# Optimization experiments

Measured on AMD Instinct MI355X. Metric: run time of the kernel, lower is better.

## Reference

```python
import jax, jax.numpy as jnp
import numpy as np

N_EMBD = 1024
N_HEAD = 16
B, T = 4, 2048


def setup_inputs() -> dict:
    key = jax.random.key(0)
    ks = jax.random.split(key, 9)
    s = 1.0 / np.sqrt(N_EMBD)
    def lin(k):
        kw, kb = jax.random.split(k)
        W = jax.random.uniform(kw, (N_EMBD, N_EMBD), jnp.float32, -s, s)
        b = jax.random.uniform(kb, (N_EMBD,), jnp.float32, -s, s)
        return W, b
    Wq, bq = lin(ks[0])
    Wk, bk = lin(ks[1])
    Wv, bv = lin(ks[2])
    Wc, bc = lin(ks[3])
    x = jax.random.normal(ks[4], (B, T, N_EMBD), jnp.float32)
    return {"x": x, "Wq": Wq, "bq": bq, "Wk": Wk, "bk": bk,
            "Wv": Wv, "bv": bv, "Wc": Wc, "bc": bc}


def reference(x, Wq, bq, Wk, bk, Wv, bv, Wc, bc):
    Bsz, Tlen, C = x.shape
    hd = C // N_HEAD  # head dim
    # projections (torch Linear: x @ W.T + b)
    q = x @ Wq.T + bq
    k = x @ Wk.T + bk
    v = x @ Wv.T + bv
    # [B, H, T, hd]
    q = q.reshape(Bsz, Tlen, N_HEAD, hd).transpose(0, 2, 1, 3)
    k = k.reshape(Bsz, Tlen, N_HEAD, hd).transpose(0, 2, 1, 3)
    v = v.reshape(Bsz, Tlen, N_HEAD, hd).transpose(0, 2, 1, 3)
    scale = 1.0 / np.sqrt(hd).astype(np.float32)
    att = jnp.einsum('bhqd,bhkd->bhqk', q, k) * scale  # [B,H,T,T]
    causal = jnp.tril(jnp.ones((Tlen, Tlen), dtype=bool))
    att = jnp.where(causal[None, None, :, :], att, -jnp.inf)
    att = jax.nn.softmax(att, axis=-1)
    y = jnp.einsum('bhqk,bhkd->bhqd', att, v)  # [B,H,T,hd]
    y = y.transpose(0, 2, 1, 3).reshape(Bsz, Tlen, C)
    return y @ Wc.T + bc
```

## Files before the change

kernel.cpp:

```cpp
#include <hip/hip_runtime.h>
#include <hip/hip_bf16.h>

typedef __bf16 bf16x8 __attribute__((ext_vector_type(8)));
typedef float f32x4 __attribute__((ext_vector_type(4)));
typedef unsigned short u16;
typedef u16 u16x8 __attribute__((ext_vector_type(8)));
typedef unsigned int u32;
typedef u32 u32x4 __attribute__((ext_vector_type(4)));

#define N_EMBD 1024
#define NH 16
#define HD 64
#define BZ 4
#define TZ 2048
#define QSCALE 0.18033688011f

template<bool B> struct BoolC { static constexpr bool value = B; };

__device__ __forceinline__ u16 f2bf(float f) {
    return __builtin_bit_cast(u16, (__bf16)f);
}

__device__ __forceinline__ void gload16(const void* g, void* l) {
    __builtin_amdgcn_global_load_lds(
        (const __attribute__((address_space(1))) void*)g,
        (__attribute__((address_space(3))) void*)l, 16, 0, 0);
}

__global__ void cvt_all(const float* __restrict__ x,  const float* __restrict__ Wq,
                        const float* __restrict__ Wk, const float* __restrict__ Wv,
                        const float* __restrict__ Wc, u16* __restrict__ xb,
                        u16* __restrict__ wqkv, u16* __restrict__ wcb) {
    const int blk = blockIdx.x;
    const float* src; u16* dst; int base; float scale = 1.0f;
    if (blk < 8192)       { src = x;  dst = xb;             base = blk; }
    else if (blk < 9216)  { src = Wq; dst = wqkv;           base = blk - 8192; scale = QSCALE; }
    else if (blk < 10240) { src = Wk; dst = wqkv + 1048576; base = blk - 9216; }
    else if (blk < 11264) { src = Wv; dst = wqkv + 2097152; base = blk - 10240; }
    else                  { src = Wc; dst = wcb;            base = blk - 11264; }
    const int i = base * 256 + threadIdx.x;
    float4 f = ((const float4*)src)[i];
    ushort4 o;
    o.x = f2bf(f.x * scale); o.y = f2bf(f.y * scale);
    o.z = f2bf(f.z * scale); o.w = f2bf(f.w * scale);
    ((ushort4*)dst)[i] = o;
}

template<int EPI>
__global__ __launch_bounds__(512, 2) void gemm_bt(
    const u16* __restrict__ A, const u16* __restrict__ Bm,
    const float* __restrict__ b0, const float* __restrict__ b1, const float* __restrict__ b2,
    void* __restrict__ Cout, int K) {
    __shared__ __align__(16) u16 Ash[6 * 8192];
    __shared__ __align__(16) u16 Bsh[6 * 4096];

    const int tid = threadIdx.x;
    const int lane = tid & 63, wid = tid >> 6;
    const int wm = wid >> 1, wn = wid & 1;
    const int m0 = blockIdx.x * 256, n0 = blockIdx.y * 128;
    const int r = lane & 15, g = lane >> 4;

    f32x4 acc[4][4] = {};

    const int p0 = tid >> 3;
    const int ci = tid & 7;
    const int cl = ci ^ (p0 & 7);
    const int trow = 2 * p0 + (cl >> 2);
    const int colb = (cl & 3) * 8;
    const u16* aS = A + (long)(m0 + trow) * K + colb;
    const u16* bS = Bm + (long)(n0 + trow) * K + colb;
    const long rowskip = (long)128 * K;
    const int ldst = tid * 8;

    auto STAGE = [&](int sig, int kq) {
        const u16* spA = aS + kq * 32;
        gload16(spA, &Ash[sig * 8192 + ldst]);
        gload16(spA + rowskip, &Ash[sig * 8192 + 4096 + ldst]);
        gload16(bS + kq * 32, &Bsh[sig * 4096 + ldst]);
    };

    const int xa = (((((r & 1) << 2) | g) ^ (r >> 1)) << 4);
    const int arow0 = wm * 32 + (r >> 1);
    const int brow0 = wn * 32 + (r >> 1);
    auto RD = [&](const u16* base, int prow) -> bf16x8 {
        return *(const bf16x8*)((const char*)base + prow * 128 + xa);
    };

    bf16x8 fa0[4], fb0[4], fa1[4], fb1[4];

    auto READF = [&](int rho, bf16x8* fa, bf16x8* fb) {
#pragma unroll
        for (int m = 0; m < 4; ++m) fa[m] = RD(&Ash[rho * 8192], arow0 + m * 8);
#pragma unroll
        for (int n = 0; n < 4; ++n) fb[n] = RD(&Bsh[rho * 4096], brow0 + n * 8);
    };
    auto MM = [&](bf16x8* fa, bf16x8* fb) {
        __builtin_amdgcn_s_setprio(1);
#pragma unroll
        for (int m = 0; m < 4; ++m)
#pragma unroll
            for (int n = 0; n < 4; ++n)
                acc[m][n] = __builtin_amdgcn_mfma_f32_16x16x32_bf16(fa[m], fb[n], acc[m][n], 0, 0, 0);
        __builtin_amdgcn_s_setprio(0);
    };
    auto BAR = [&] {
        asm volatile("" ::: "memory");
        __builtin_amdgcn_s_barrier();
        asm volatile("" ::: "memory");
    };

    const int nph = K >> 5;

    STAGE(0, 0); STAGE(1, 1); STAGE(2, 2); STAGE(3, 3); STAGE(4, 4);
    asm volatile("s_waitcnt vmcnt(9)" ::: "memory");
    BAR();
    READF(0, fa0, fb0);

    int rho = 0;
    for (int p = 0; p + 2 < nph; p += 2) {
        const int rho1 = rho + 1;
        const int rho2 = (rho + 2 == 6) ? 0 : rho + 2;
        const int sigE = (rho == 0) ? 5 : rho - 1;
        const int kqE = (p + 5 < nph) ? p + 5 : 0;
        const int kqO = (p + 6 < nph) ? p + 6 : 0;
        BAR();
        READF(rho1, fa1, fb1);
        STAGE(sigE, kqE);
        MM(fa0, fb0);
        asm volatile("s_waitcnt vmcnt(9)" ::: "memory");
        BAR();
        READF(rho2, fa0, fb0);
        STAGE(rho, kqO);
        MM(fa1, fb1);
        asm volatile("s_waitcnt vmcnt(9)" ::: "memory");
        rho = rho2;
    }
    {
        const int rho1 = rho + 1;
        const int sigE = (rho == 0) ? 5 : rho - 1;
        BAR();
        READF(rho1, fa1, fb1);
        STAGE(sigE, 0);
        MM(fa0, fb0);
        asm volatile("s_waitcnt vmcnt(9)" ::: "memory");
    }
    MM(fa1, fb1);
    asm volatile("s_waitcnt vmcnt(0)" ::: "memory");

    const long planeSz = (long)BZ * NH * TZ * HD;
    if constexpr (EPI == 0) {
        const int proj = n0 >> 10;
        u16* outp = (u16*)Cout;
        if (proj == 2) {
            const int bi = (m0 + wm * 64) >> 11;
#pragma unroll
            for (int n = 0; n < 4; ++n) {
                const int rr = (n0 & 1023) + wn * 64 + n * 16 + r;
                const int h = rr >> 6, d = rr & 63;
                const float bias = b2[rr];
                u16* vcol = outp + 2 * planeSz + (((long)bi * NH + h) * HD + d) * TZ;
#pragma unroll
                for (int m = 0; m < 4; ++m) {
                    const int t0 = (m0 + wm * 64 + m * 16 + g * 4) & 2047;
                    ushort4 o;
                    o.x = f2bf(acc[m][n][0] + bias);
                    o.y = f2bf(acc[m][n][1] + bias);
                    o.z = f2bf(acc[m][n][2] + bias);
                    o.w = f2bf(acc[m][n][3] + bias);
                    *(ushort4*)(vcol + t0) = o;
                }
            }
        } else {
#pragma unroll
            for (int n = 0; n < 4; ++n) {
                const int rr = (n0 & 1023) + wn * 64 + n * 16 + r;
                const int h = rr >> 6, d = rr & 63;
                float bias = (proj == 0 ? b0 : b1)[rr];
                if (proj == 0) bias *= QSCALE;
                const long pbase = (long)proj * planeSz + d;
#pragma unroll
                for (int m = 0; m < 4; ++m)
#pragma unroll
                    for (int reg = 0; reg < 4; ++reg) {
                        const int row = m0 + wm * 64 + m * 16 + g * 4 + reg;
                        const int bi = row >> 11, t = row & 2047;
                        outp[pbase + ((long)bi * NH + h) * (TZ * HD) + (long)t * HD] =
                            f2bf(acc[m][n][reg] + bias);
                    }
            }
        }
    } else {
        float* outp = (float*)Cout;
#pragma unroll
        for (int n = 0; n < 4; ++n) {
            const int col = n0 + wn * 64 + n * 16 + r;
            const float bias = b0[col];
#pragma unroll
            for (int m = 0; m < 4; ++m)
#pragma unroll
                for (int reg = 0; reg < 4; ++reg) {
                    const int row = m0 + wm * 64 + m * 16 + g * 4 + reg;
                    outp[(long)row * N_EMBD + col] = acc[m][n][reg] + bias;
                }
        }
    }
}

__device__ __forceinline__ bf16x8 lds_swz8(const u16* base, int row, int colByte) {
    return *(const bf16x8*)((const char*)base + row * 128 + (colByte ^ ((row & 7) << 4)));
}

__global__ __launch_bounds__(512, 2) void attn_fwd(const u16* __restrict__ qkv, u16* __restrict__ yb) {
    const int i = blockIdx.x;
    const int xcd = i & 7, slot = i >> 3;
    const int bh = xcd + 8 * (slot & 7);
    const int pr = slot >> 3;
    const int b = bh >> 4, h = bh & 15;
    const int tid = threadIdx.x, lane = tid & 63, w = tid >> 6;
    const int r = lane & 15, g = lane >> 4;

    __shared__ __align__(16) u16 Ksh[2][64 * 64];
    __shared__ __align__(16) u16 Vsh[2][64 * 64];

    const long planeSz = (long)BZ * NH * TZ * HD;
    const long bhoff = ((long)b * NH + h) * (long)TZ * HD;
    const u16* qp = qkv + bhoff;
    const u16* kp = qkv + planeSz + bhoff;
    const u16* vTp = qkv + 2 * planeSz + bhoff;

    const int rr8 = tid >> 3;
    const int ss = ((tid & 7) ^ (rr8 & 7)) * 8;

#pragma unroll 1
    for (int it = 0; it < 2; ++it) {
        const int qblk = it ? pr : (15 - pr);
        const int q0 = qblk * 128;
        const int nkt = 2 * qblk + 2;

        bf16x8 qf[2];
        {
            const int q = q0 + w * 16 + r;
#pragma unroll
            for (int ks = 0; ks < 2; ++ks)
                qf[ks] = *(const bf16x8*)(qp + (long)q * HD + ks * 32 + g * 8);
        }

        f32x4 yacc[4] = {};
        float mrun = -__builtin_inff(), lpart = 0.f;

        gload16(kp + (long)rr8 * HD + ss, &Ksh[0][tid * 8]);
        gload16(vTp + (long)rr8 * TZ + ss, &Vsh[0][tid * 8]);

        auto tile = [&](int kt, auto maskc) {
            constexpr bool MASK = decltype(maskc)::value;
            const int cur = kt & 1;
            const int k0 = kt * 64;
            if (kt + 1 < nkt) {
                const int k0n = k0 + 64;
                gload16(kp + (long)(k0n + rr8) * HD + ss, &Ksh[cur ^ 1][tid * 8]);
                gload16(vTp + (long)rr8 * TZ + k0n + ss, &Vsh[cur ^ 1][tid * 8]);
                asm volatile("s_waitcnt vmcnt(2)" ::: "memory");
            } else {
                asm volatile("s_waitcnt vmcnt(0)" ::: "memory");
            }
            __builtin_amdgcn_s_barrier();
            asm volatile("" ::: "memory");

            f32x4 sac[4] = {};
#pragma unroll
            for (int ks = 0; ks < 2; ++ks) {
                bf16x8 kf[4];
#pragma unroll
                for (int nk = 0; nk < 4; ++nk)
                    kf[nk] = lds_swz8(Ksh[cur], nk * 16 + r, ks * 64 + g * 16);
                __builtin_amdgcn_s_setprio(1);
#pragma unroll
                for (int nk = 0; nk < 4; ++nk)
                    sac[nk] = __builtin_amdgcn_mfma_f32_16x16x32_bf16(kf[nk], qf[ks], sac[nk], 0, 0, 0);
                __builtin_amdgcn_s_setprio(0);
            }

            if constexpr (MASK) {
                const int q = q0 + w * 16 + r;
#pragma unroll
                for (int nk = 0; nk < 4; ++nk)
#pragma unroll
                    for (int reg = 0; reg < 4; ++reg) {
                        const int k = k0 + nk * 16 + g * 4 + reg;
                        sac[nk][reg] = (k > q) ? -__builtin_inff() : sac[nk][reg];
                    }
            }
            float pmax;
            {
                float t0 = fmaxf(fmaxf(sac[0][0], sac[0][1]), fmaxf(sac[0][2], sac[0][3]));
                float t1 = fmaxf(fmaxf(sac[1][0], sac[1][1]), fmaxf(sac[1][2], sac[1][3]));
                float t2 = fmaxf(fmaxf(sac[2][0], sac[2][1]), fmaxf(sac[2][2], sac[2][3]));
                float t3 = fmaxf(fmaxf(sac[3][0], sac[3][1]), fmaxf(sac[3][2], sac[3][3]));
                pmax = fmaxf(fmaxf(t0, t1), fmaxf(t2, t3));
            }
            if (__any(pmax > mrun + 8.0f)) {
                float mx = pmax;
                mx = fmaxf(mx, __shfl_xor(mx, 16));
                mx = fmaxf(mx, __shfl_xor(mx, 32));
                const float mnew = fmaxf(mrun, mx);
                const float corr = __builtin_amdgcn_exp2f(mrun - mnew);
                lpart *= corr;
#pragma unroll
                for (int nd = 0; nd < 4; ++nd)
                    yacc[nd] *= corr;
                mrun = mnew;
            }
            float rs[4];
#pragma unroll
            for (int nk = 0; nk < 4; ++nk) {
                float p0 = __builtin_amdgcn_exp2f(sac[nk][0] - mrun);
                float p1 = __builtin_amdgcn_exp2f(sac[nk][1] - mrun);
                float p2 = __builtin_amdgcn_exp2f(sac[nk][2] - mrun);
                float p3 = __builtin_amdgcn_exp2f(sac[nk][3] - mrun);
                sac[nk][0] = p0; sac[nk][1] = p1;
                sac[nk][2] = p2; sac[nk][3] = p3;
                rs[nk] = (p0 + p1) + (p2 + p3);
            }
            lpart += (rs[0] + rs[1]) + (rs[2] + rs[3]);

            u32 wv[4][2];
#pragma unroll
            for (int nk = 0; nk < 4; ++nk)
#pragma unroll
                for (int j2 = 0; j2 < 2; ++j2)
                    asm("v_cvt_pk_bf16_f32 %0, %1, %2"
                        : "=v"(wv[nk][j2])
                        : "v"(sac[nk][2 * j2]), "v"(sac[nk][2 * j2 + 1]));
            u32 pw[2][4];
#pragma unroll
            for (int ks = 0; ks < 2; ++ks) {
                u32 a0 = wv[2 * ks][0], b0 = wv[2 * ks + 1][0];
                u32 a1 = wv[2 * ks][1], b1 = wv[2 * ks + 1][1];
                asm("v_permlane32_swap_b32 %0, %1" : "+v"(a0), "+v"(b0));
                asm("v_permlane32_swap_b32 %0, %1" : "+v"(a1), "+v"(b1));
                asm("v_permlane16_swap_b32 %0, %1" : "+v"(a0), "+v"(b0));
                asm("v_permlane16_swap_b32 %0, %1" : "+v"(a1), "+v"(b1));
                pw[ks][0] = a0; pw[ks][1] = a1;
                pw[ks][2] = b0; pw[ks][3] = b1;
            }

#pragma unroll
            for (int ks = 0; ks < 2; ++ks) {
                bf16x8 vf[4];
#pragma unroll
                for (int nd = 0; nd < 4; ++nd)
                    vf[nd] = lds_swz8(Vsh[cur], nd * 16 + r, ks * 64 + g * 16);
                const u32x4 pwv = { pw[ks][0], pw[ks][1], pw[ks][2], pw[ks][3] };
                const bf16x8 pb = __builtin_bit_cast(bf16x8, pwv);
                __builtin_amdgcn_s_setprio(1);
#pragma unroll
                for (int nd = 0; nd < 4; ++nd)
                    yacc[nd] = __builtin_amdgcn_mfma_f32_16x16x32_bf16(vf[nd], pb, yacc[nd], 0, 0, 0);
                __builtin_amdgcn_s_setprio(0);
            }

            asm volatile("" ::: "memory");
            __builtin_amdgcn_s_barrier();
            asm volatile("" ::: "memory");
        };

        for (int kt = 0; kt + 2 < nkt; ++kt) tile(kt, BoolC<false>{});
        tile(nkt - 2, BoolC<true>{});
        tile(nkt - 1, BoolC<true>{});

        {
            float l = lpart;
            l += __shfl_xor(l, 16);
            l += __shfl_xor(l, 32);
            const float inv = 1.f / l;
            const int q = q0 + w * 16 + r;
            u16* orow = yb + ((long)b * TZ + q) * N_EMBD + h * HD;
#pragma unroll
            for (int nd = 0; nd < 4; ++nd) {
                ushort4 o;
                o.x = f2bf(yacc[nd][0] * inv);
                o.y = f2bf(yacc[nd][1] * inv);
                o.z = f2bf(yacc[nd][2] * inv);
                o.w = f2bf(yacc[nd][3] * inv);
                *(ushort4*)(orow + nd * 16 + g * 4) = o;
            }
        }
    }
}

extern "C" void kernel_launch(void* const* d_in, const int* in_sizes, int n_in,
                              void* d_out, int out_size, void* d_ws, size_t ws_size,
                              hipStream_t stream) {
    const float* x  = (const float*)d_in[0];
    const float* Wq = (const float*)d_in[1];
    const float* bq = (const float*)d_in[2];
    const float* Wk = (const float*)d_in[3];
    const float* bk = (const float*)d_in[4];
    const float* Wv = (const float*)d_in[5];
    const float* bv = (const float*)d_in[6];
    const float* Wc = (const float*)d_in[7];
    const float* bc = (const float*)d_in[8];

    char* ws = (char*)d_ws;
    u16* xb   = (u16*)(ws);
    u16* wqkv = (u16*)(ws + 16777216);
    u16* wcb  = (u16*)(ws + 23068672);
    u16* qkv  = (u16*)(ws + 25165824);
    u16* yb   = (u16*)(ws + 75497472);

    cvt_all<<<12288, 256, 0, stream>>>(x, Wq, Wk, Wv, Wc, xb, wqkv, wcb);

    gemm_bt<0><<<dim3(32, 24), 512, 0, stream>>>(xb, wqkv, bq, bk, bv, (void*)qkv, 1024);

    attn_fwd<<<512, 512, 0, stream>>>(qkv, yb);

    gemm_bt<1><<<dim3(32, 8), 512, 0, stream>>>(yb, wcb, bc, nullptr, nullptr, d_out, 1024);
}
```

Measured before the change: 161.5 us.

## Use a 256x256-tile GEMM kernel for the fused QKV projection

Adds a new bf16 MFMA GEMM variant with 256x256 output tiles, a four-stage LDS ring buffer with prefetch distance two, and eight waves in a 2x4 layout each computing 128x64. The QKV projection launch switches to it, halving the grid along N. The larger tile raises arithmetic intensity per LDS byte and cuts redundant global loads of A. In exchange, occupancy drops to one block per CU and the 384-block grid may leave an uneven final wave.

```diff
diff --git a/kernel.cpp b/kernel.cpp
--- a/kernel.cpp
+++ b/kernel.cpp
@@ -44,6 +44,146 @@
     o.x = f2bf(f.x * scale); o.y = f2bf(f.y * scale);
     o.z = f2bf(f.z * scale); o.w = f2bf(f.w * scale);
     ((ushort4*)dst)[i] = o;
+}
+
+template<int EPI>
+__global__ __launch_bounds__(512, 1) void gemm256_bt(
+    const u16* __restrict__ A, const u16* __restrict__ Bm,
+    const float* __restrict__ b0, const float* __restrict__ b1, const float* __restrict__ b2,
+    void* __restrict__ Cout, int K) {
+    __shared__ __align__(16) u16 Ash[4 * 8192];
+    __shared__ __align__(16) u16 Bsh[4 * 8192];
+
+    const int tid = threadIdx.x;
+    const int lane = tid & 63, wid = tid >> 6;
+    const int wm = wid >> 2, wn = wid & 3;
+    const int m0 = blockIdx.x * 256, n0 = blockIdx.y * 256;
+    const int r = lane & 15, g = lane >> 4;
+
+    f32x4 acc[8][4] = {};
+
+    const int p0 = tid >> 3;
+    const int ci = tid & 7;
+    const int cl = ci ^ (p0 & 7);
+    const int trow = 2 * p0 + (cl >> 2);
+    const int colb = (cl & 3) * 8;
+    const u16* aS = A + (long)(m0 + trow) * K + colb;
+    const u16* bS = Bm + (long)(n0 + trow) * K + colb;
+    const long rowskip = (long)128 * K;
+    const int ldst = tid * 8;
+
+    auto STAGE = [&](int sig, int kq) {
+        const u16* spA = aS + kq * 32;
+        u16* dA = Ash + sig * 8192 + ldst;
+        gload16(spA, dA);
+        gload16(spA + rowskip, dA + 4096);
+        const u16* spB = bS + kq * 32;
+        u16* dB = Bsh + sig * 8192 + ldst;
+        gload16(spB, dB);
+        gload16(spB + rowskip, dB + 4096);
+    };
+
+    const int xa = (((((r & 1) << 2) | g) ^ (r >> 1)) << 4);
+    const int arow0 = wm * 64 + (r >> 1);
+    const int brow0 = wn * 32 + (r >> 1);
+    auto RD = [&](const u16* base, int prow) -> bf16x8 {
+        return *(const bf16x8*)((const char*)base + prow * 128 + xa);
+    };
+
+    const int nph = K >> 5;
+
+    STAGE(0, 0); STAGE(1, 1);
+    asm volatile("s_waitcnt vmcnt(4)" ::: "memory");
+    __builtin_amdgcn_s_barrier();
+    asm volatile("" ::: "memory");
+
+#pragma unroll 1
+    for (int p = 0; p < nph; ++p) {
+        const int rho = p & 3, tgt = (p + 2) & 3;
+        const int kq = (p + 2 < nph) ? p + 2 : 0;
+        bf16x8 fa[8], fb[4];
+        const u16* Ab = Ash + rho * 8192;
+        const u16* Bb = Bsh + rho * 8192;
+#pragma unroll
+        for (int m = 0; m < 8; ++m) fa[m] = RD(Ab, arow0 + m * 8);
+#pragma unroll
+        for (int n = 0; n < 4; ++n) fb[n] = RD(Bb, brow0 + n * 8);
+        STAGE(tgt, kq);
+        asm volatile("" ::: "memory");
+        __builtin_amdgcn_s_barrier();
+        asm volatile("s_waitcnt lgkmcnt(0)" ::: "memory");
+        __builtin_amdgcn_sched_barrier(0);
+        __builtin_amdgcn_s_setprio(1);
+#pragma unroll
+        for (int m = 0; m < 8; ++m)
+#pragma unroll
+            for (int n = 0; n < 4; ++n)
+                acc[m][n] = __builtin_amdgcn_mfma_f32_16x16x32_bf16(fa[m], fb[n], acc[m][n], 0, 0, 0);
+        __builtin_amdgcn_s_setprio(0);
+        asm volatile("s_waitcnt vmcnt(4)" ::: "memory");
+        asm volatile("" ::: "memory");
+        __builtin_amdgcn_s_barrier();
+        asm volatile("" ::: "memory");
+    }
+    asm volatile("s_waitcnt vmcnt(0)" ::: "memory");
+
+    const long planeSz = (long)BZ * NH * TZ * HD;
+    if constexpr (EPI == 0) {
+        const int proj = n0 >> 10;
+        u16* outp = (u16*)Cout;
+        if (proj == 2) {
+            const int bi = (m0 + wm * 128) >> 11;
+#pragma unroll
+            for (int n = 0; n < 4; ++n) {
+                const int rr = (n0 & 1023) + wn * 64 + n * 16 + r;
+                const int h = rr >> 6, d = rr & 63;
+                const float bias = b2[rr];
+                u16* vcol = outp + 2 * planeSz + (((long)bi * NH + h) * HD + d) * TZ;
+#pragma unroll
+                for (int mf = 0; mf < 8; ++mf) {
+                    const int t0 = (m0 + wm * 128 + mf * 16 + g * 4) & 2047;
+                    ushort4 o;
+                    o.x = f2bf(acc[mf][n][0] + bias);
+                    o.y = f2bf(acc[mf][n][1] + bias);
+                    o.z = f2bf(acc[mf][n][2] + bias);
+                    o.w = f2bf(acc[mf][n][3] + bias);
+                    *(ushort4*)(vcol + t0) = o;
+                }
+            }
+        } else {
+#pragma unroll
+            for (int n = 0; n < 4; ++n) {
+                const int rr = (n0 & 1023) + wn * 64 + n * 16 + r;
+                const int h = rr >> 6, d = rr & 63;
+                float bias = (proj == 0 ? b0 : b1)[rr];
+                if (proj == 0) bias *= QSCALE;
+                const long pbase = (long)proj * planeSz + d;
+#pragma unroll
+                for (int mf = 0; mf < 8; ++mf)
+#pragma unroll
+                    for (int reg = 0; reg < 4; ++reg) {
+                        const int row = m0 + wm * 128 + mf * 16 + g * 4 + reg;
+                        const int bi = row >> 11, t = row & 2047;
+                        outp[pbase + ((long)bi * NH + h) * (TZ * HD) + (long)t * HD] =
+                            f2bf(acc[mf][n][reg] + bias);
+                    }
+            }
+        }
+    } else {
+        float* outp = (float*)Cout;
+#pragma unroll
+        for (int n = 0; n < 4; ++n) {
+            const int col = n0 + wn * 64 + n * 16 + r;
+            const float bias = b0[col];
+#pragma unroll
+            for (int mf = 0; mf < 8; ++mf)
+#pragma unroll
+                for (int reg = 0; reg < 4; ++reg) {
+                    const int row = m0 + wm * 128 + mf * 16 + g * 4 + reg;
+                    outp[(long)row * N_EMBD + col] = acc[mf][n][reg] + bias;
+                }
+        }
+    }
 }
 
 template<int EPI>
@@ -410,7 +550,7 @@
 
     cvt_all<<<12288, 256, 0, stream>>>(x, Wq, Wk, Wv, Wc, xb, wqkv, wcb);
 
-    gemm_bt<0><<<dim3(32, 24), 512, 0, stream>>>(xb, wqkv, bq, bk, bv, (void*)qkv, 1024);
+    gemm256_bt<0><<<dim3(32, 12), 512, 0, stream>>>(xb, wqkv, bq, bk, bv, (void*)qkv, 1024);
 
     attn_fwd<<<512, 512, 0, stream>>>(qkv, yb);
 
```

New measurement: 168.9 us. 4.6% more time.

## Give each attention wave two 16-row query fragments and halve block size

Applied to the files above, without the earlier changes.

The attention kernel now launches 256 threads per block instead of 512. Each wave handles 32 query rows as two 16-row fragments, so every K and V fragment read from LDS feeds two MFMAs. Each thread now issues two K and two V async loads per tile to fill the same 64x64 shared tiles. The goal is to cut LDS read traffic and barrier cost per unit of compute, at the price of more registers per thread (doubled accumulators and score tiles) and fewer waves to hide latency.

```diff
diff --git a/kernel.cpp b/kernel.cpp
--- a/kernel.cpp
+++ b/kernel.cpp
@@ -210,7 +210,7 @@
     return *(const bf16x8*)((const char*)base + row * 128 + (colByte ^ ((row & 7) << 4)));
 }
 
-__global__ __launch_bounds__(512, 2) void attn_fwd(const u16* __restrict__ qkv, u16* __restrict__ yb) {
+__global__ __launch_bounds__(256, 2) void attn_fwd(const u16* __restrict__ qkv, u16* __restrict__ yb) {
     const int i = blockIdx.x;
     const int xcd = i & 7, slot = i >> 3;
     const int bh = xcd + 8 * (slot & 7);
@@ -228,28 +228,33 @@
     const u16* kp = qkv + planeSz + bhoff;
     const u16* vTp = qkv + 2 * planeSz + bhoff;
 
-    const int rr8 = tid >> 3;
-    const int ss = ((tid & 7) ^ (rr8 & 7)) * 8;
+    const int rr8 = tid >> 3, scb = tid & 7;
 
 #pragma unroll 1
     for (int it = 0; it < 2; ++it) {
         const int qblk = it ? pr : (15 - pr);
         const int q0 = qblk * 128;
         const int nkt = 2 * qblk + 2;
-
-        bf16x8 qf[2];
-        {
-            const int q = q0 + w * 16 + r;
+        const int qa = q0 + w * 32 + r;
+
+        bf16x8 qf[2][2];
+#pragma unroll
+        for (int f = 0; f < 2; ++f)
 #pragma unroll
             for (int ks = 0; ks < 2; ++ks)
-                qf[ks] = *(const bf16x8*)(qp + (long)q * HD + ks * 32 + g * 8);
+                qf[f][ks] = *(const bf16x8*)(qp + (long)(qa + f * 16) * HD + ks * 32 + g * 8);
+
+        f32x4 yacc[4][2] = {};
+        float mrun[2] = { -__builtin_inff(), -__builtin_inff() };
+        float lpart[2] = { 0.f, 0.f };
+
+#pragma unroll
+        for (int h2 = 0; h2 < 2; ++h2) {
+            const int kk = h2 * 32 + rr8;
+            const int ss = (scb ^ (kk & 7)) * 8;
+            gload16(kp + (long)kk * HD + ss, &Ksh[0][h2 * 2048 + tid * 8]);
+            gload16(vTp + (long)kk * TZ + ss, &Vsh[0][h2 * 2048 + tid * 8]);
         }
-
-        f32x4 yacc[4] = {};
-        float mrun = -__builtin_inff(), lpart = 0.f;
-
-        gload16(kp + (long)rr8 * HD + ss, &Ksh[0][tid * 8]);
-        gload16(vTp + (long)rr8 * TZ + ss, &Vsh[0][tid * 8]);
 
         auto tile = [&](int kt, auto maskc) {
             constexpr bool MASK = decltype(maskc)::value;
@@ -257,16 +262,21 @@
             const int k0 = kt * 64;
             if (kt + 1 < nkt) {
                 const int k0n = k0 + 64;
-                gload16(kp + (long)(k0n + rr8) * HD + ss, &Ksh[cur ^ 1][tid * 8]);
-                gload16(vTp + (long)rr8 * TZ + k0n + ss, &Vsh[cur ^ 1][tid * 8]);
-                asm volatile("s_waitcnt vmcnt(2)" ::: "memory");
+#pragma unroll
+                for (int h2 = 0; h2 < 2; ++h2) {
+                    const int kk = h2 * 32 + rr8;
+                    const int ss = (scb ^ (kk & 7)) * 8;
+                    gload16(kp + (long)(k0n + kk) * HD + ss, &Ksh[cur ^ 1][h2 * 2048 + tid * 8]);
+                    gload16(vTp + (long)kk * TZ + k0n + ss, &Vsh[cur ^ 1][h2 * 2048 + tid * 8]);
+                }
+                asm volatile("s_waitcnt vmcnt(4)" ::: "memory");
             } else {
                 asm volatile("s_waitcnt vmcnt(0)" ::: "memory");
             }
             __builtin_amdgcn_s_barrier();
             asm volatile("" ::: "memory");
 
-            f32x4 sac[4] = {};
+            f32x4 sac[4][2] = {};
 #pragma unroll
             for (int ks = 0; ks < 2; ++ks) {
                 bf16x8 kf[4];
@@ -276,72 +286,81 @@
                 __builtin_amdgcn_s_setprio(1);
 #pragma unroll
                 for (int nk = 0; nk < 4; ++nk)
-                    sac[nk] = __builtin_amdgcn_mfma_f32_16x16x32_bf16(kf[nk], qf[ks], sac[nk], 0, 0, 0);
+#pragma unroll
+                    for (int f = 0; f < 2; ++f)
+                        sac[nk][f] = __builtin_amdgcn_mfma_f32_16x16x32_bf16(kf[nk], qf[f][ks], sac[nk][f], 0, 0, 0);
                 __builtin_amdgcn_s_setprio(0);
             }
 
             if constexpr (MASK) {
-                const int q = q0 + w * 16 + r;
+#pragma unroll
+                for (int f = 0; f < 2; ++f) {
+                    const int qm = qa + f * 16;
+#pragma unroll
+                    for (int nk = 0; nk < 4; ++nk)
+#pragma unroll
+                        for (int reg = 0; reg < 4; ++reg) {
+                            const int k = k0 + nk * 16 + g * 4 + reg;
+                            sac[nk][f][reg] = (k > qm) ? -__builtin_inff() : sac[nk][f][reg];
+                        }
+                }
+            }
+
+            u32 pwa[2][2][4];
+#pragma unroll
+            for (int f = 0; f < 2; ++f) {
+                float pmax;
+                {
+                    float t0 = fmaxf(fmaxf(sac[0][f][0], sac[0][f][1]), fmaxf(sac[0][f][2], sac[0][f][3]));
+                    float t1 = fmaxf(fmaxf(sac[1][f][0], sac[1][f][1]), fmaxf(sac[1][f][2], sac[1][f][3]));
+                    float t2 = fmaxf(fmaxf(sac[2][f][0], sac[2][f][1]), fmaxf(sac[2][f][2], sac[2][f][3]));
+                    float t3 = fmaxf(fmaxf(sac[3][f][0], sac[3][f][1]), fmaxf(sac[3][f][2], sac[3][f][3]));
+                    pmax = fmaxf(fmaxf(t0, t1), fmaxf(t2, t3));
+                }
+                if (__any(pmax > mrun[f] + 8.0f)) {
+                    float mx = pmax;
+                    mx = fmaxf(mx, __shfl_xor(mx, 16));
+                    mx = fmaxf(mx, __shfl_xor(mx, 32));
+                    const float mnew = fmaxf(mrun[f], mx);
+                    const float corr = __builtin_amdgcn_exp2f(mrun[f] - mnew);
+                    lpart[f] *= corr;
+#pragma unroll
+                    for (int nd = 0; nd < 4; ++nd)
+                        yacc[nd][f] *= corr;
+                    mrun[f] = mnew;
+                }
+                float rs[4];
+#pragma unroll
+                for (int nk = 0; nk < 4; ++nk) {
+                    float p0 = __builtin_amdgcn_exp2f(sac[nk][f][0] - mrun[f]);
+                    float p1 = __builtin_amdgcn_exp2f(sac[nk][f][1] - mrun[f]);
+                    float p2 = __builtin_amdgcn_exp2f(sac[nk][f][2] - mrun[f]);
+                    float p3 = __builtin_amdgcn_exp2f(sac[nk][f][3] - mrun[f]);
+                    sac[nk][f][0] = p0; sac[nk][f][1] = p1;
+                    sac[nk][f][2] = p2; sac[nk][f][3] = p3;
+                    rs[nk] = (p0 + p1) + (p2 + p3);
+                }
+                lpart[f] += (rs[0] + rs[1]) + (rs[2] + rs[3]);
+
+                u32 wv[4][2];
 #pragma unroll
                 for (int nk = 0; nk < 4; ++nk)
 #pragma unroll
-                    for (int reg = 0; reg < 4; ++reg) {
-                        const int k = k0 + nk * 16 + g * 4 + reg;
-                        sac[nk][reg] = (k > q) ? -__builtin_inff() : sac[nk][reg];
-                    }
-            }
-            float pmax;
-            {
-                float t0 = fmaxf(fmaxf(sac[0][0], sac[0][1]), fmaxf(sac[0][2], sac[0][3]));
-                float t1 = fmaxf(fmaxf(sac[1][0], sac[1][1]), fmaxf(sac[1][2], sac[1][3]));
-                float t2 = fmaxf(fmaxf(sac[2][0], sac[2][1]), fmaxf(sac[2][2], sac[2][3]));
-                float t3 = fmaxf(fmaxf(sac[3][0], sac[3][1]), fmaxf(sac[3][2], sac[3][3]));
-                pmax = fmaxf(fmaxf(t0, t1), fmaxf(t2, t3));
-            }
-            if (__any(pmax > mrun + 8.0f)) {
-                float mx = pmax;
-                mx = fmaxf(mx, __shfl_xor(mx, 16));
-                mx = fmaxf(mx, __shfl_xor(mx, 32));
-                const float mnew = fmaxf(mrun, mx);
-                const float corr = __builtin_amdgcn_exp2f(mrun - mnew);
-                lpart *= corr;
-#pragma unroll
-                for (int nd = 0; nd < 4; ++nd)
-                    yacc[nd] *= corr;
-                mrun = mnew;
-            }
-            float rs[4];
-#pragma unroll
-            for (int nk = 0; nk < 4; ++nk) {
-                float p0 = __builtin_amdgcn_exp2f(sac[nk][0] - mrun);
-                float p1 = __builtin_amdgcn_exp2f(sac[nk][1] - mrun);
-                float p2 = __builtin_amdgcn_exp2f(sac[nk][2] - mrun);
-                float p3 = __builtin_amdgcn_exp2f(sac[nk][3] - mrun);
-                sac[nk][0] = p0; sac[nk][1] = p1;
-                sac[nk][2] = p2; sac[nk][3] = p3;
-                rs[nk] = (p0 + p1) + (p2 + p3);
-            }
-            lpart += (rs[0] + rs[1]) + (rs[2] + rs[3]);
-
-            u32 wv[4][2];
-#pragma unroll
-            for (int nk = 0; nk < 4; ++nk)
-#pragma unroll
-                for (int j2 = 0; j2 < 2; ++j2)
-                    asm("v_cvt_pk_bf16_f32 %0, %1, %2"
-                        : "=v"(wv[nk][j2])
-                        : "v"(sac[nk][2 * j2]), "v"(sac[nk][2 * j2 + 1]));
-            u32 pw[2][4];
-#pragma unroll
-            for (int ks = 0; ks < 2; ++ks) {
-                u32 a0 = wv[2 * ks][0], b0 = wv[2 * ks + 1][0];
-                u32 a1 = wv[2 * ks][1], b1 = wv[2 * ks + 1][1];
-                asm("v_permlane32_swap_b32 %0, %1" : "+v"(a0), "+v"(b0));
-                asm("v_permlane32_swap_b32 %0, %1" : "+v"(a1), "+v"(b1));
-                asm("v_permlane16_swap_b32 %0, %1" : "+v"(a0), "+v"(b0));
-                asm("v_permlane16_swap_b32 %0, %1" : "+v"(a1), "+v"(b1));
-                pw[ks][0] = a0; pw[ks][1] = a1;
-                pw[ks][2] = b0; pw[ks][3] = b1;
+                    for (int j2 = 0; j2 < 2; ++j2)
+                        asm("v_cvt_pk_bf16_f32 %0, %1, %2"
+                            : "=v"(wv[nk][j2])
+                            : "v"(sac[nk][f][2 * j2]), "v"(sac[nk][f][2 * j2 + 1]));
+#pragma unroll
+                for (int ks = 0; ks < 2; ++ks) {
+                    u32 a0 = wv[2 * ks][0], c0 = wv[2 * ks + 1][0];
+                    u32 a1 = wv[2 * ks][1], c1 = wv[2 * ks + 1][1];
+                    asm("v_permlane32_swap_b32 %0, %1" : "+v"(a0), "+v"(c0));
+                    asm("v_permlane32_swap_b32 %0, %1" : "+v"(a1), "+v"(c1));
+                    asm("v_permlane16_swap_b32 %0, %1" : "+v"(a0), "+v"(c0));
+                    asm("v_permlane16_swap_b32 %0, %1" : "+v"(a1), "+v"(c1));
+                    pwa[f][ks][0] = a0; pwa[f][ks][1] = a1;
+                    pwa[f][ks][2] = c0; pwa[f][ks][3] = c1;
+                }
             }
 
 #pragma unroll
@@ -350,12 +369,15 @@
 #pragma unroll
                 for (int nd = 0; nd < 4; ++nd)
                     vf[nd] = lds_swz8(Vsh[cur], nd * 16 + r, ks * 64 + g * 16);
-                const u32x4 pwv = { pw[ks][0], pw[ks][1], pw[ks][2], pw[ks][3] };
-                const bf16x8 pb = __builtin_bit_cast(bf16x8, pwv);
                 __builtin_amdgcn_s_setprio(1);
 #pragma unroll
                 for (int nd = 0; nd < 4; ++nd)
-                    yacc[nd] = __builtin_amdgcn_mfma_f32_16x16x32_bf16(vf[nd], pb, yacc[nd], 0, 0, 0);
+#pragma unroll
+                    for (int f = 0; f < 2; ++f) {
+                        const u32x4 pwv = { pwa[f][ks][0], pwa[f][ks][1], pwa[f][ks][2], pwa[f][ks][3] };
+                        const bf16x8 pb = __builtin_bit_cast(bf16x8, pwv);
+                        yacc[nd][f] = __builtin_amdgcn_mfma_f32_16x16x32_bf16(vf[nd], pb, yacc[nd][f], 0, 0, 0);
+                    }
                 __builtin_amdgcn_s_setprio(0);
             }
 
@@ -368,20 +390,20 @@
         tile(nkt - 2, BoolC<true>{});
         tile(nkt - 1, BoolC<true>{});
 
-        {
-            float l = lpart;
+#pragma unroll
+        for (int f = 0; f < 2; ++f) {
+            float l = lpart[f];
             l += __shfl_xor(l, 16);
             l += __shfl_xor(l, 32);
             const float inv = 1.f / l;
-            const int q = q0 + w * 16 + r;
-            u16* orow = yb + ((long)b * TZ + q) * N_EMBD + h * HD;
+            u16* orow = yb + ((long)b * TZ + (qa + f * 16)) * N_EMBD + h * HD;
 #pragma unroll
             for (int nd = 0; nd < 4; ++nd) {
                 ushort4 o;
-                o.x = f2bf(yacc[nd][0] * inv);
-                o.y = f2bf(yacc[nd][1] * inv);
-                o.z = f2bf(yacc[nd][2] * inv);
-                o.w = f2bf(yacc[nd][3] * inv);
+                o.x = f2bf(yacc[nd][f][0] * inv);
+                o.y = f2bf(yacc[nd][f][1] * inv);
+                o.z = f2bf(yacc[nd][f][2] * inv);
+                o.w = f2bf(yacc[nd][f][3] * inv);
                 *(ushort4*)(orow + nd * 16 + g * 4) = o;
             }
         }
@@ -412,7 +434,7 @@
 
     gemm_bt<0><<<dim3(32, 24), 512, 0, stream>>>(xb, wqkv, bq, bk, bv, (void*)qkv, 1024);
 
-    attn_fwd<<<512, 512, 0, stream>>>(qkv, yb);
+    attn_fwd<<<512, 256, 0, stream>>>(qkv, yb);
 
     gemm_bt<1><<<dim3(32, 8), 512, 0, stream>>>(yb, wcb, bc, nullptr, nullptr, d_out, 1024);
 }
```

Result: no change. 163.4 us (+1.2%).
